# Kernel optimization log

Hardware: AMD Instinct MI355X
Metric: run time of the kernel (lower is better)

The kernel has to match this reference:

```python
import jax, jax.numpy as jnp
import numpy as np

# The conv3d with a fixed one-hot [5,1,1,3,3] filter is a gather of 5 spatial
# shifts of the (edge-padded) volume. Kernel hot positions (ky,kx):
#   ch0:(0,0) ch1:(1,1) ch2:(2,2) ch3:(2,0) ch4:(0,2)
_OFFSETS = ((0, 0), (1, 1), (2, 2), (2, 0), (0, 2))


def setup_inputs() -> dict:
    key = jax.random.key(0)
    prob_volume = jax.random.normal(key, (2, 1, 48, 256, 512), dtype=jnp.float32)
    return {"prob_volume": prob_volume}


def reference(prob_volume) -> jnp.ndarray:
    B, C, D, H, W = prob_volume.shape  # C == 1
    # ReplicationPad3d((1,1,1,1,0,0)): pad W and H by 1 with edge values, D by 0.
    p = jnp.pad(prob_volume, ((0, 0), (0, 0), (0, 0), (1, 1), (1, 1)), mode="edge")
    # Each output channel is a shifted window of the padded volume.
    out = jnp.concatenate(
        [p[:, :, :, ky:ky + H, kx:kx + W] for (ky, kx) in _OFFSETS], axis=1
    )  # [B, 5, D, H, W]
    return out
```

## Files before the change

kernel.cpp:

```cpp
#include <hip/hip_runtime.h>


typedef float f32x4 __attribute__((ext_vector_type(4)));

constexpr int D = 48, H = 256, W = 512;
constexpr int W4 = W / 4;
constexpr int HB = 8;

__device__ __forceinline__ void nt_store4(float* p, float a, float b, float c, float d) {
    f32x4 v = {a, b, c, d};
    __builtin_nontemporal_store(v, reinterpret_cast<f32x4*>(p));
}

__global__ __launch_bounds__(256) void prop_kernel(
    const float* __restrict__ in, float* __restrict__ out) {
    const int w4   = threadIdx.x & (W4 - 1);
    const int hgrp = threadIdx.x >> 7;
    const int lane = threadIdx.x & 63;

    int blk = blockIdx.x;
    const int h16 = blk & 15;
    blk >>= 4;
    const int d = blk % D;
    const int b = blk / D;

    const int h0 = h16 * (2 * HB) + hgrp * HB;
    const int w0 = w4 * 4;

    const float* base = in + (b * D + d) * (H * W);

    float4 v[HB + 2];
    float  L[HB + 2], R[HB + 2];
    #pragma unroll
    for (int i = 0; i < HB + 2; ++i) {
        int r = h0 - 1 + i;
        r = r < 0 ? 0 : (r > H - 1 ? H - 1 : r);
        const float* row = base + r * W;
        float4 t = *reinterpret_cast<const float4*>(row + w0);
        float l  = __shfl_up(t.w, 1);
        float rr = __shfl_down(t.x, 1);
        if (w4 == 0)          l  = t.x;
        else if (lane == 0)   l  = row[w0 - 1];
        if (w4 == W4 - 1)     rr = t.w;
        else if (lane == 63)  rr = row[w0 + 4];
        v[i] = t; L[i] = l; R[i] = rr;
    }

    const int planeDHW = D * H * W;
    float* o0 = out + ((b * 5) * D + d) * (H * W) + h0 * W + w0;

    #pragma unroll
    for (int j = 0; j < HB; ++j) {
        const int m = j;
        nt_store4(o0 + j * W, L[m], v[m].x, v[m].y, v[m].z);
    }
    #pragma unroll
    for (int j = 0; j < HB; ++j) {
        const int c = j + 1;
        nt_store4(o0 + planeDHW + j * W, v[c].x, v[c].y, v[c].z, v[c].w);
    }
    #pragma unroll
    for (int j = 0; j < HB; ++j) {
        const int p = j + 2;
        nt_store4(o0 + 2 * planeDHW + j * W, v[p].y, v[p].z, v[p].w, R[p]);
    }
    #pragma unroll
    for (int j = 0; j < HB; ++j) {
        const int p = j + 2;
        nt_store4(o0 + 3 * planeDHW + j * W, L[p], v[p].x, v[p].y, v[p].z);
    }
    #pragma unroll
    for (int j = 0; j < HB; ++j) {
        const int m = j;
        nt_store4(o0 + 4 * planeDHW + j * W, v[m].y, v[m].z, v[m].w, R[m]);
    }
}

extern "C" void kernel_launch(void* const* d_in, const int* in_sizes, int n_in,
                              void* d_out, int out_size, void* d_ws, size_t ws_size,
                              hipStream_t stream) {
    const float* in = (const float*)d_in[0];
    float* out = (float*)d_out;

    const int grid = 2 * D * (H / (2 * HB));
    prop_kernel<<<grid, 256, 0, stream>>>(in, out);
}
```

Measured before the change: 53.54 us.

## Software-pipeline row-window loads across four iterations per block with double buffering

Each block now handles 32 rows in four iterations of 4 rows per half-block, with a double-buffered register window. The next window's loads are issued before the current window is shuffled and stored, so loads overlap stores. The grid shrinks by half and more halo rows are re-read (6 loaded per 4 output rows instead of 10 per 8), adding some input traffic.

```diff
diff --git a/kernel.cpp b/kernel.cpp
--- a/kernel.cpp
+++ b/kernel.cpp
@@ -5,11 +5,66 @@
 
 constexpr int D = 48, H = 256, W = 512;
 constexpr int W4 = W / 4;
-constexpr int HB = 8;
+constexpr int HB = 4;
+constexpr int NIT = 4;
+constexpr int WIN = HB + 2;
 
 __device__ __forceinline__ void nt_store4(float* p, float a, float b, float c, float d) {
     f32x4 v = {a, b, c, d};
     __builtin_nontemporal_store(v, reinterpret_cast<f32x4*>(p));
+}
+
+__device__ __forceinline__ void load_win(const float* __restrict__ base,
+                                         int h0, int w0, float4 (&v)[WIN]) {
+    #pragma unroll
+    for (int i = 0; i < WIN; ++i) {
+        int r = h0 - 1 + i;
+        r = r < 0 ? 0 : (r > H - 1 ? H - 1 : r);
+        v[i] = *reinterpret_cast<const float4*>(base + r * W + w0);
+    }
+}
+
+__device__ __forceinline__ void finish_store(const float* __restrict__ base,
+                                             float* __restrict__ obase,
+                                             int planeDHW, int h0, int w0,
+                                             int w4, int lane,
+                                             const float4 (&v)[WIN]) {
+    float L[WIN], R[WIN];
+    #pragma unroll
+    for (int i = 0; i < WIN; ++i) {
+        int r = h0 - 1 + i;
+        r = r < 0 ? 0 : (r > H - 1 ? H - 1 : r);
+        const float* row = base + r * W;
+        float l  = __shfl_up(v[i].w, 1);
+        float rr = __shfl_down(v[i].x, 1);
+        if (w4 == 0)          l  = v[i].x;
+        else if (lane == 0)   l  = row[w0 - 1];
+        if (w4 == W4 - 1)     rr = v[i].w;
+        else if (lane == 63)  rr = row[w0 + 4];
+        L[i] = l; R[i] = rr;
+    }
+
+    float* o0 = obase + h0 * W;
+    #pragma unroll
+    for (int j = 0; j < HB; ++j) {
+        nt_store4(o0 + j * W, L[j], v[j].x, v[j].y, v[j].z);
+    }
+    #pragma unroll
+    for (int j = 0; j < HB; ++j) {
+        nt_store4(o0 + planeDHW + j * W, v[j+1].x, v[j+1].y, v[j+1].z, v[j+1].w);
+    }
+    #pragma unroll
+    for (int j = 0; j < HB; ++j) {
+        nt_store4(o0 + 2 * planeDHW + j * W, v[j+2].y, v[j+2].z, v[j+2].w, R[j+2]);
+    }
+    #pragma unroll
+    for (int j = 0; j < HB; ++j) {
+        nt_store4(o0 + 3 * planeDHW + j * W, L[j+2], v[j+2].x, v[j+2].y, v[j+2].z);
+    }
+    #pragma unroll
+    for (int j = 0; j < HB; ++j) {
+        nt_store4(o0 + 4 * planeDHW + j * W, v[j].y, v[j].z, v[j].w, R[j]);
+    }
 }
 
 __global__ __launch_bounds__(256) void prop_kernel(
@@ -19,60 +74,30 @@
     const int lane = threadIdx.x & 63;
 
     int blk = blockIdx.x;
-    const int h16 = blk & 15;
-    blk >>= 4;
+    const int hq = blk & 7;
+    blk >>= 3;
     const int d = blk % D;
     const int b = blk / D;
 
-    const int h0 = h16 * (2 * HB) + hgrp * HB;
     const int w0 = w4 * 4;
+    const float* base = in + (b * D + d) * (H * W);
+    const int planeDHW = D * H * W;
+    float* obase = out + (b * 5 * D + d) * (H * W) + w0;
 
-    const float* base = in + (b * D + d) * (H * W);
-
-    float4 v[HB + 2];
-    float  L[HB + 2], R[HB + 2];
-    #pragma unroll
-    for (int i = 0; i < HB + 2; ++i) {
-        int r = h0 - 1 + i;
-        r = r < 0 ? 0 : (r > H - 1 ? H - 1 : r);
-        const float* row = base + r * W;
-        float4 t = *reinterpret_cast<const float4*>(row + w0);
-        float l  = __shfl_up(t.w, 1);
-        float rr = __shfl_down(t.x, 1);
-        if (w4 == 0)          l  = t.x;
-        else if (lane == 0)   l  = row[w0 - 1];
-        if (w4 == W4 - 1)     rr = t.w;
-        else if (lane == 63)  rr = row[w0 + 4];
-        v[i] = t; L[i] = l; R[i] = rr;
-    }
-
-    const int planeDHW = D * H * W;
-    float* o0 = out + ((b * 5) * D + d) * (H * W) + h0 * W + w0;
+    float4 vA[WIN], vB[WIN];
+    load_win(base, hq * 32 + hgrp * HB, w0, vA);
 
     #pragma unroll
-    for (int j = 0; j < HB; ++j) {
-        const int m = j;
-        nt_store4(o0 + j * W, L[m], v[m].x, v[m].y, v[m].z);
-    }
-    #pragma unroll
-    for (int j = 0; j < HB; ++j) {
-        const int c = j + 1;
-        nt_store4(o0 + planeDHW + j * W, v[c].x, v[c].y, v[c].z, v[c].w);
-    }
-    #pragma unroll
-    for (int j = 0; j < HB; ++j) {
-        const int p = j + 2;
-        nt_store4(o0 + 2 * planeDHW + j * W, v[p].y, v[p].z, v[p].w, R[p]);
-    }
-    #pragma unroll
-    for (int j = 0; j < HB; ++j) {
-        const int p = j + 2;
-        nt_store4(o0 + 3 * planeDHW + j * W, L[p], v[p].x, v[p].y, v[p].z);
-    }
-    #pragma unroll
-    for (int j = 0; j < HB; ++j) {
-        const int m = j;
-        nt_store4(o0 + 4 * planeDHW + j * W, v[m].y, v[m].z, v[m].w, R[m]);
+    for (int it = 0; it < NIT; ++it) {
+        const int h0c = hq * 32 + it * 8 + hgrp * HB;
+        const int h0n = h0c + 8;
+        if ((it & 1) == 0) {
+            if (it < NIT - 1) load_win(base, h0n, w0, vB);
+            finish_store(base, obase, planeDHW, h0c, w0, w4, lane, vA);
+        } else {
+            if (it < NIT - 1) load_win(base, h0n, w0, vA);
+            finish_store(base, obase, planeDHW, h0c, w0, w4, lane, vB);
+        }
     }
 }
 
@@ -82,6 +107,6 @@
     const float* in = (const float*)d_in[0];
     float* out = (float*)d_out;
 
-    const int grid = 2 * D * (H / (2 * HB));
+    const int grid = 2 * D * (H / (2 * HB * NIT));
     prop_kernel<<<grid, 256, 0, stream>>>(in, out);
 }
```

Result: slower. 69.30 us (+29.4%).

## Give each wave a full row with 8 floats per lane and swizzle block order

Applied to the files above, without the earlier changes.

Each thread now loads 8 contiguous floats (two 16-byte vectors) so that one 64-lane wave covers a whole 512-wide row. The left and right neighbours then come entirely from wave shuffles, with clamping only at lanes 0 and 63, which removes the extra scalar global loads at wave boundaries. Blocks now cover 32 rows using 4 waves of 8 rows each, the grid is halved, and block indices are permuted in groups of 8, likely to spread consecutive blocks across XCDs or memory channels. The cost is more registers per thread and fewer blocks in flight.

```diff
diff --git a/kernel.cpp b/kernel.cpp
--- a/kernel.cpp
+++ b/kernel.cpp
@@ -4,46 +4,46 @@
 typedef float f32x4 __attribute__((ext_vector_type(4)));
 
 constexpr int D = 48, H = 256, W = 512;
-constexpr int W4 = W / 4;
 constexpr int HB = 8;
+constexpr int WIN = HB + 2;
 
-__device__ __forceinline__ void nt_store4(float* p, float a, float b, float c, float d) {
-    f32x4 v = {a, b, c, d};
+__device__ __forceinline__ void nt_store(float* p, f32x4 v) {
     __builtin_nontemporal_store(v, reinterpret_cast<f32x4*>(p));
 }
 
 __global__ __launch_bounds__(256) void prop_kernel(
     const float* __restrict__ in, float* __restrict__ out) {
-    const int w4   = threadIdx.x & (W4 - 1);
-    const int hgrp = threadIdx.x >> 7;
     const int lane = threadIdx.x & 63;
+    const int wv   = threadIdx.x >> 6;
 
-    int blk = blockIdx.x;
-    const int h16 = blk & 15;
-    blk >>= 4;
-    const int d = blk % D;
-    const int b = blk / D;
+    int lb = (blockIdx.x & 7) * 96 + (blockIdx.x >> 3);
+    const int h32 = lb & 7;
+    lb >>= 3;
+    const int d = lb % D;
+    const int b = lb / D;
 
-    const int h0 = h16 * (2 * HB) + hgrp * HB;
-    const int w0 = w4 * 4;
+    const int h0 = h32 * 32 + wv * HB;
+    const int w0 = lane * 8;
 
     const float* base = in + (b * D + d) * (H * W);
 
-    float4 v[HB + 2];
-    float  L[HB + 2], R[HB + 2];
+    f32x4 q0[WIN], q1[WIN];
     #pragma unroll
-    for (int i = 0; i < HB + 2; ++i) {
+    for (int i = 0; i < WIN; ++i) {
         int r = h0 - 1 + i;
         r = r < 0 ? 0 : (r > H - 1 ? H - 1 : r);
-        const float* row = base + r * W;
-        float4 t = *reinterpret_cast<const float4*>(row + w0);
-        float l  = __shfl_up(t.w, 1);
-        float rr = __shfl_down(t.x, 1);
-        if (w4 == 0)          l  = t.x;
-        else if (lane == 0)   l  = row[w0 - 1];
-        if (w4 == W4 - 1)     rr = t.w;
-        else if (lane == 63)  rr = row[w0 + 4];
-        v[i] = t; L[i] = l; R[i] = rr;
+        const float* row = base + r * W + w0;
+        q0[i] = *reinterpret_cast<const f32x4*>(row);
+        q1[i] = *reinterpret_cast<const f32x4*>(row + 4);
+    }
+
+    float L[WIN], R[WIN];
+    #pragma unroll
+    for (int i = 0; i < WIN; ++i) {
+        float l  = __shfl_up(q1[i].w, 1);
+        float rr = __shfl_down(q0[i].x, 1);
+        L[i] = (lane == 0)  ? q0[i].x : l;
+        R[i] = (lane == 63) ? q1[i].w : rr;
     }
 
     const int planeDHW = D * H * W;
@@ -52,27 +52,39 @@
     #pragma unroll
     for (int j = 0; j < HB; ++j) {
         const int m = j;
-        nt_store4(o0 + j * W, L[m], v[m].x, v[m].y, v[m].z);
+        f32x4 a = {L[m], q0[m].x, q0[m].y, q0[m].z};
+        f32x4 c = {q0[m].w, q1[m].x, q1[m].y, q1[m].z};
+        nt_store(o0 + j * W, a);
+        nt_store(o0 + j * W + 4, c);
     }
     #pragma unroll
     for (int j = 0; j < HB; ++j) {
-        const int c = j + 1;
-        nt_store4(o0 + planeDHW + j * W, v[c].x, v[c].y, v[c].z, v[c].w);
+        nt_store(o0 + planeDHW + j * W, q0[j + 1]);
+        nt_store(o0 + planeDHW + j * W + 4, q1[j + 1]);
     }
     #pragma unroll
     for (int j = 0; j < HB; ++j) {
         const int p = j + 2;
-        nt_store4(o0 + 2 * planeDHW + j * W, v[p].y, v[p].z, v[p].w, R[p]);
+        f32x4 a = {q0[p].y, q0[p].z, q0[p].w, q1[p].x};
+        f32x4 c = {q1[p].y, q1[p].z, q1[p].w, R[p]};
+        nt_store(o0 + 2 * planeDHW + j * W, a);
+        nt_store(o0 + 2 * planeDHW + j * W + 4, c);
     }
     #pragma unroll
     for (int j = 0; j < HB; ++j) {
         const int p = j + 2;
-        nt_store4(o0 + 3 * planeDHW + j * W, L[p], v[p].x, v[p].y, v[p].z);
+        f32x4 a = {L[p], q0[p].x, q0[p].y, q0[p].z};
+        f32x4 c = {q0[p].w, q1[p].x, q1[p].y, q1[p].z};
+        nt_store(o0 + 3 * planeDHW + j * W, a);
+        nt_store(o0 + 3 * planeDHW + j * W + 4, c);
     }
     #pragma unroll
     for (int j = 0; j < HB; ++j) {
         const int m = j;
-        nt_store4(o0 + 4 * planeDHW + j * W, v[m].y, v[m].z, v[m].w, R[m]);
+        f32x4 a = {q0[m].y, q0[m].z, q0[m].w, q1[m].x};
+        f32x4 c = {q1[m].y, q1[m].z, q1[m].w, R[m]};
+        nt_store(o0 + 4 * planeDHW + j * W, a);
+        nt_store(o0 + 4 * planeDHW + j * W + 4, c);
     }
 }
 
@@ -82,6 +94,6 @@
     const float* in = (const float*)d_in[0];
     float* out = (float*)d_out;
 
-    const int grid = 2 * D * (H / (2 * HB));
+    const int grid = 2 * D * (H / 32);
     prop_kernel<<<grid, 256, 0, stream>>>(in, out);
 }
```

Result: slower. 166.1 us (+210.2%).
